# Optimization experiments

Measured on AMD Instinct MI355X. Metric: run time of the kernel, lower is better.

## Reference

```python
import jax, jax.numpy as jnp
import numpy as np

H, D, CR, SEL_K = 8, 64, 32, 16          # query heads, head dim, block size, top-k blocks
ROPE_DIM, THETA, WINDOW, GROUPS = 32, 10000.0, 512, 2
INTER, HID, QC = 512, 1024, 256
NEG = -1e30


def _rope_cache(t):
    half = ROPE_DIM // 2
    inv = 1.0 / (THETA ** (jnp.arange(half, dtype=jnp.float32) * 2.0 / ROPE_DIM))
    ang = jnp.arange(t, dtype=jnp.float32)[:, None] * inv[None, :]  # (t, half)
    return jnp.cos(ang), jnp.sin(ang)


def _apply_partial_rope(x, cos, sin):
    half = ROPE_DIM // 2
    x1, x2, rest = x[..., :half], x[..., half:ROPE_DIM], x[..., ROPE_DIM:]
    return jnp.concatenate([x1 * cos - x2 * sin, x1 * sin + x2 * cos, rest], -1)


def _rmsnorm(x, g, eps=1e-6):
    return x * jax.lax.rsqrt(jnp.mean(x * x, -1, keepdims=True) + eps) * g


def setup_inputs():
    key = jax.random.key(0)
    ks = jax.random.split(key, 9)
    f = lambda k, shp, s: jax.random.normal(k, shp, jnp.float32) * s
    return {
        "h": f(ks[0], (1, 2048, HID), 1.0),
        "w_qc": f(ks[1], (HID, QC), QC ** -0.5),
        "w_qup": f(ks[2], (QC, H * D), (H * D) ** -0.5),
        "w_k": f(ks[3], (HID, D), HID ** -0.5),
        "w_v": f(ks[4], (HID, D), HID ** -0.5),
        "g_qnorm": jnp.ones((D,), jnp.float32),
        "g_knorm": jnp.ones((D,), jnp.float32),
        "w_gate": f(ks[5], (D, 3), 0.05),
        "b_gate": jnp.zeros((3,), jnp.float32),
        "sink_logit": f(ks[6], (H,), 0.1),
        "w_out_group": f(ks[7], (GROUPS, (H // GROUPS) * D, INTER), 0.05),
        "w_out": f(ks[8], (GROUPS * INTER, HID), 0.03),
    }


def reference(h, w_qc, w_qup, w_k, w_v, g_qnorm, g_knorm, w_gate, b_gate,
              sink_logit, w_out_group, w_out):
    b, t, _ = h.shape
    cos, sin = _rope_cache(t)
    q = (h @ w_qc @ w_qup).reshape(b, t, H, D).transpose(0, 2, 1, 3)  # (b,H,t,D)
    q = _rmsnorm(_apply_partial_rope(q, cos, sin), g_qnorm)
    k = _rmsnorm(_apply_partial_rope(h @ w_k, cos, sin), g_knorm)      # (b,t,D)
    v = h @ w_v                                                        # (b,t,D)
    scale = 1.0 / np.sqrt(D).astype(np.float32)
    qpos = jnp.arange(t)
    sink = jnp.broadcast_to(sink_logit[None, :, None, None], (b, H, t, 1))

    # ---- compressed branch: attend over block-mean pooled K/V ----
    nb = t // CR
    kc = k[:, :nb * CR].reshape(b, nb, CR, D).mean(2)                  # (b,nb,D)
    vc = v[:, :nb * CR].reshape(b, nb, CR, D).mean(2)
    comp_valid = ((jnp.arange(nb) + 1) * CR - 1)[None, :] <= qpos[:, None]  # (t,nb)
    any_blk = comp_valid.any(-1, keepdims=True)                        # (t,1)
    safe = jnp.where(any_blk, comp_valid, True)
    sc_raw = jnp.einsum('bhqd,bnd->bhqn', q, kc) * scale
    pc = jax.nn.softmax(jnp.concatenate([jnp.where(safe, sc_raw, NEG), sink], -1), -1)
    comp_out = jnp.einsum('bhqn,bnd->bhqd', pc[..., :nb], vc)
    comp_out = jnp.where(any_blk[None, None], comp_out, 0.0)

    # ---- selective branch: top-k blocks per query, dense-masked gather-equivalent ----
    sel_sc = jnp.where(comp_valid, sc_raw, -jnp.inf)
    top_idx = jax.lax.top_k(sel_sc, min(SEL_K, nb))[1]                 # (b,H,t,K)
    sel_blocks = (top_idx[..., :, None] == jnp.arange(nb)).any(-2)     # (b,H,t,nb)
    block_of = jnp.minimum(qpos // CR, nb - 1)
    causal = qpos[:, None] >= qpos[None, :]                            # (t,t)
    in_range = qpos < nb * CR
    tok_sel = sel_blocks[..., block_of] & (causal & in_range[None, :])[None, None]
    scores_full = jnp.einsum('bhqd,bkd->bhqk', q, k) * scale           # (b,H,t,t)
    ps = jax.nn.softmax(jnp.where(tok_sel, scores_full, NEG), -1)
    sel_out = jnp.einsum('bhqk,bkd->bhqd', ps, v)

    # ---- sliding-window branch ----
    sw = causal & ((qpos[:, None] - qpos[None, :]) < WINDOW)
    pw = jax.nn.softmax(
        jnp.concatenate([jnp.where(sw[None, None], scores_full, NEG), sink], -1), -1)
    sw_out = jnp.einsum('bhqk,bkd->bhqd', pw[..., :t], v)

    # ---- learned gate over the three branches ----
    g = jax.nn.sigmoid(q @ w_gate + b_gate)                            # (b,H,t,3)
    g = g / jnp.clip(g.sum(-1, keepdims=True), 1e-6)
    mixed = g[..., 0:1] * comp_out + g[..., 1:2] * sel_out + g[..., 2:3] * sw_out

    # ---- grouped output projection ----
    x = mixed.transpose(0, 2, 1, 3).reshape(b, t, GROUPS, (H // GROUPS) * D)
    y = jnp.einsum('btgf,gfi->btgi', x, w_out_group).reshape(b, t, GROUPS * INTER)
    return y @ w_out
```

## Files before the change

### kernel.cpp

```cpp
#include <hip/hip_runtime.h>
#include <hip/hip_bf16.h>
#include <float.h>
#include <math.h>

typedef __hip_bfloat16 bf16;
typedef float v2f __attribute__((ext_vector_type(2)));

#define NEGBIG (-1e30f)

__device__ __forceinline__ float ldv(const float* p, int i) { return p[i]; }

__device__ __forceinline__ float wave_sum(float v) {
#pragma unroll
  for (int off = 32; off; off >>= 1) v += __shfl_xor(v, off, 64);
  return v;
}
__device__ __forceinline__ float wave_max(float v) {
#pragma unroll
  for (int off = 32; off; off >>= 1) v = fmaxf(v, __shfl_xor(v, off, 64));
  return v;
}

__device__ __forceinline__ float rdlane(float v, int l) {
  return __uint_as_float(__builtin_amdgcn_readlane(__float_as_uint(v), l));
}

template <int L0>
__device__ __forceinline__ void pv16(const float* __restrict__ vp, float e,
                                     float& a0, float& a1, float& a2, float& a3) {
#pragma unroll
  for (int t = 0; t < 16; t += 4) {
    float p0 = rdlane(e, L0 + t + 0);
    float p1 = rdlane(e, L0 + t + 1);
    float p2 = rdlane(e, L0 + t + 2);
    float p3 = rdlane(e, L0 + t + 3);
    a0 += p0 * vp[(t + 0) * 64];
    a1 += p1 * vp[(t + 1) * 64];
    a2 += p2 * vp[(t + 2) * 64];
    a3 += p3 * vp[(t + 3) * 64];
  }
}

__device__ __forceinline__ float qk_dot(const float4* __restrict__ qr,
                                        const float4* __restrict__ kp) {
  v2f d01 = {0.f, 0.f}, d23 = {0.f, 0.f};
#pragma unroll 1
  for (int i = 0; i < 16; i += 2) {
    float4 q0 = qr[i],     k0 = kp[i * 32];
    float4 q1 = qr[i + 1], k1 = kp[i * 32 + 32];
    d01 += (v2f){q0.x, q0.y} * (v2f){k0.x, k0.y};
    d23 += (v2f){q0.z, q0.w} * (v2f){k0.z, k0.w};
    d01 += (v2f){q1.x, q1.y} * (v2f){k1.x, k1.y};
    d23 += (v2f){q1.z, q1.w} * (v2f){k1.z, k1.w};
  }
  v2f d = d01 + d23;
  return d.x + d.y;
}

__device__ __forceinline__ void gemm_core(
    const float* __restrict__ A, const float* __restrict__ B, float* __restrict__ C,
    int K, int lda, int ldb, int ldc, int row0, int col0)
{
  __shared__ __align__(16) float As[2][16][68];
  __shared__ __align__(16) float Bs[2][16][68];
  const int tid = threadIdx.x;
  const int tx = tid & 15, ty = tid >> 4;
  const int ar = tid >> 2;
  const int ak = (tid & 3) * 4;
  const int bk = tid >> 4;
  const int bc = (tid & 15) * 4;

  const int nk = K >> 4;
  float4 a4 = *reinterpret_cast<const float4*>(&A[(row0 + ar) * lda + ak]);
  float4 b4 = *reinterpret_cast<const float4*>(&B[bk * ldb + col0 + bc]);
  {
    As[0][ak + 0][ar] = a4.x; As[0][ak + 1][ar] = a4.y;
    As[0][ak + 2][ar] = a4.z; As[0][ak + 3][ar] = a4.w;
    *reinterpret_cast<float4*>(&Bs[0][bk][bc]) = b4;
  }

  v2f acc01[4] = {};
  v2f acc23[4] = {};
  for (int t = 0; t < nk; ++t) {
    const int cur = t & 1;
    if (t + 1 < nk) {
      int k0 = (t + 1) * 16;
      a4 = *reinterpret_cast<const float4*>(&A[(row0 + ar) * lda + k0 + ak]);
      b4 = *reinterpret_cast<const float4*>(&B[(k0 + bk) * ldb + col0 + bc]);
    }
    __syncthreads();
#pragma unroll
    for (int kk = 0; kk < 16; ++kk) {
      float4 av = *reinterpret_cast<const float4*>(&As[cur][kk][ty * 4]);
      float4 bv = *reinterpret_cast<const float4*>(&Bs[cur][kk][tx * 4]);
      v2f b01; b01.x = bv.x; b01.y = bv.y;
      v2f b23; b23.x = bv.z; b23.y = bv.w;
      float a[4] = {av.x, av.y, av.z, av.w};
#pragma unroll
      for (int i = 0; i < 4; ++i) {
        v2f as; as.x = a[i]; as.y = a[i];
        acc01[i] += as * b01;
        acc23[i] += as * b23;
      }
    }
    if (t + 1 < nk) {
      const int nxt = cur ^ 1;
      As[nxt][ak + 0][ar] = a4.x; As[nxt][ak + 1][ar] = a4.y;
      As[nxt][ak + 2][ar] = a4.z; As[nxt][ak + 3][ar] = a4.w;
      *reinterpret_cast<float4*>(&Bs[nxt][bk][bc]) = b4;
    }
  }
#pragma unroll
  for (int i = 0; i < 4; ++i) {
    float4 o = make_float4(acc01[i].x, acc01[i].y, acc23[i].x, acc23[i].y);
    *reinterpret_cast<float4*>(&C[(row0 + ty * 4 + i) * ldc + col0 + tx * 4]) = o;
  }
}

__global__ __launch_bounds__(256) void gemm_tile(
    const float* __restrict__ A, const float* __restrict__ B, float* __restrict__ C,
    int M, int N, int K, int lda, int ldb, int ldc)
{
  gemm_core(A, B, C, K, lda, ldb, ldc, blockIdx.y * 64, blockIdx.x * 64);
}

__global__ __launch_bounds__(256) void gemm_qckv(
    const float* __restrict__ h, const float* __restrict__ w_qc,
    const float* __restrict__ w_k, const float* __restrict__ w_v,
    float* __restrict__ hc, float* __restrict__ kb, float* __restrict__ vb)
{
  const int x = blockIdx.x;
  if (x < 4) {
    gemm_core(h, w_qc, hc, 1024, 1024, 256, 256, blockIdx.y * 64, x * 64);
  } else if (x == 4) {
    gemm_core(h, w_k, kb, 1024, 1024, 64, 64, blockIdx.y * 64, 0);
  } else {
    gemm_core(h, w_v, vb, 1024, 1024, 64, 64, blockIdx.y * 64, 0);
  }
}

__global__ __launch_bounds__(256) void gemm_dual(
    const float* __restrict__ A0, const float* __restrict__ A1,
    const float* __restrict__ B0, const float* __restrict__ B1,
    float* __restrict__ C0, float* __restrict__ C1,
    int K, int lda, int ldb, int ldc, int nx)
{
  const bool second = (int)blockIdx.x >= nx;
  const float* A = second ? A1 : A0;
  const float* B = second ? B1 : B0;
  float* C = second ? C1 : C0;
  const int bx = second ? (blockIdx.x - nx) : blockIdx.x;
  gemm_core(A, B, C, K, lda, ldb, ldc, blockIdx.y * 64, bx * 64);
}

__global__ __launch_bounds__(256) void rope_table_kernel(float* __restrict__ ct,
                                                         float* __restrict__ st) {
  int tid = blockIdx.x * 256 + threadIdx.x;
  if (tid >= 2048 * 16) return;
  int pos = tid >> 4, i = tid & 15;
  double ang = (double)pos * pow(10000.0, -(double)i / 16.0);
  ct[tid] = (float)cos(ang);
  st[tid] = (float)sin(ang);
}

__device__ __forceinline__ void rope_body(
    float* __restrict__ x, const float* __restrict__ g, int rows, int posShift,
    float* __restrict__ kS, const float* __restrict__ ct, const float* __restrict__ st,
    int bx)
{
  const int lane = threadIdx.x & 63;
  const int wid = threadIdx.x >> 6;
  const int r = bx * 4 + wid;
  if (r >= rows) return;
  const int pos = r >> posShift;
  float val = x[r * 64 + lane];
  float p = __shfl_xor(val, 16, 64);
  float out = val;
  if (lane < 32) {
    int i = lane & 15;
    float cc = ct[pos * 16 + i], ss = st[pos * 16 + i];
    out = (lane < 16) ? (val * cc - p * ss) : (p * ss + val * cc);
  }
  float ms = wave_sum(out * out) * (1.0f / 64.0f);
  float rn = rsqrtf(ms + 1e-6f);
  float res = out * rn * ldv(g, lane);
  x[r * 64 + lane] = res;
  if (kS) {
    int f4 = (r >> 5) * 512 + (lane >> 2) * 32 + (r & 31);
    kS[f4 * 4 + (lane & 3)] = res;
  }
}

__global__ __launch_bounds__(256) void rope_rms_fused(
    float* __restrict__ qx, float* __restrict__ kx,
    const float* __restrict__ gq, const float* __restrict__ gk,
    float* __restrict__ kS, const float* __restrict__ ct, const float* __restrict__ st)
{
  const int bx = blockIdx.x;
  if (bx < 4096) rope_body(qx, gq, 16384, 3, nullptr, ct, st, bx);
  else           rope_body(kx, gk, 2048, 0, kS, ct, st, bx - 4096);
}

__global__ void compress_kernel(const float* __restrict__ k, const float* __restrict__ v,
                                float* __restrict__ kcT4, float* __restrict__ vc)
{
  const int n = blockIdx.x;
  const int d = threadIdx.x;
  float sk = 0.f, sv = 0.f;
  for (int j = 0; j < 32; ++j) {
    sk += k[(n * 32 + j) * 64 + d];
    sv += v[(n * 32 + j) * 64 + d];
  }
  kcT4[(d >> 2) * 256 + n * 4 + (d & 3)] = sk * (1.0f / 32.0f);
  vc[n * 64 + d] = sv * (1.0f / 32.0f);
}

__global__ __launch_bounds__(512) void attn_kernel(
    const float* __restrict__ q, const float* __restrict__ kS, const float* __restrict__ vbuf,
    const float* __restrict__ kcT4, const float* __restrict__ vc,
    const float* __restrict__ w_gate, const float* __restrict__ b_gate,
    const float* __restrict__ sink, float* __restrict__ mixed)
{
  __shared__ __align__(16) float4 stgK[1024];
  __shared__ __align__(16) float stgV[4096];
  __shared__ __align__(16) float shq[8][64];
  __shared__ int shsel[8][16];
  const int tid = threadIdx.x;
  const int lane = tid & 63;
  const int wid = tid >> 6;
  const int qpos = 2047 - blockIdx.x;
  const int h = wid;
  const int r = qpos * 8 + h;
  const float scale = 0.125f;

  float qv = q[r * 64 + lane];
  shq[wid][lane] = qv;

  float z0 = qv * ldv(w_gate, lane * 3 + 0);
  float z1 = qv * ldv(w_gate, lane * 3 + 1);
  float z2 = qv * ldv(w_gate, lane * 3 + 2);
  z0 = wave_sum(z0) + ldv(b_gate, 0);
  z1 = wave_sum(z1) + ldv(b_gate, 1);
  z2 = wave_sum(z2) + ldv(b_gate, 2);
  float ga0 = 1.f / (1.f + expf(-z0));
  float ga1 = 1.f / (1.f + expf(-z1));
  float ga2 = 1.f / (1.f + expf(-z2));
  float gs = fmaxf(ga0 + ga1 + ga2, 1e-6f);
  float ginv = 1.f / gs;
  ga0 *= ginv; ga1 *= ginv; ga2 *= ginv;

  const float4* qr = reinterpret_cast<const float4*>(&shq[wid][0]);
  const float4* ks4 = reinterpret_cast<const float4*>(kS);
  const float4* kct = reinterpret_cast<const float4*>(kcT4);
  const float snk = ldv(sink, h);
  const int nv = (qpos + 1) >> 5;


  float sc;
  {
    float d0 = 0.f, d1 = 0.f;
#pragma unroll 1
    for (int i = 0; i < 16; i += 2) {
      float4 q0 = qr[i],     k0 = kct[i * 64 + lane];
      float4 q1 = qr[i + 1], k1 = kct[(i + 1) * 64 + lane];
      d0 += q0.x * k0.x + q0.z * k0.z;
      d1 += q0.y * k0.y + q0.w * k0.w;
      d0 += q1.x * k1.x + q1.z * k1.z;
      d1 += q1.y * k1.y + q1.w * k1.w;
    }
    sc = (d0 + d1) * scale;
  }

  float comp_out = 0.f;
  if (nv > 0) {
    float scomp = (lane < nv) ? sc : NEGBIG;
    float m = fmaxf(wave_max(scomp), snk);
    float e = (lane < nv) ? expf(sc - m) : 0.f;
    float S = wave_sum(e) + expf(snk - m);
    float pn = e / S;
    const float* vcp = vc + lane;
    float c0 = 0.f, c1 = 0.f, c2 = 0.f, c3 = 0.f;
    pv16<0>(vcp, pn, c0, c1, c2, c3);
    pv16<16>(vcp + 1024, pn, c0, c1, c2, c3);
    pv16<32>(vcp + 2048, pn, c0, c1, c2, c3);
    pv16<48>(vcp + 3072, pn, c0, c1, c2, c3);
    comp_out = (c0 + c1) + (c2 + c3);
  }

  {
    float selv = (lane < nv) ? sc : -FLT_MAX;
#pragma unroll
    for (int it = 0; it < 16; ++it) {
      float bv = selv; int bi = lane;
#pragma unroll
      for (int off = 32; off; off >>= 1) {
        float ov = __shfl_xor(bv, off, 64);
        int oi = __shfl_xor(bi, off, 64);
        if (ov > bv || (ov == bv && oi < bi)) { bv = ov; bi = oi; }
      }
      if (lane == 0) shsel[wid][it] = bi;
      if (lane == bi) selv = -INFINITY;
    }
  }

  float M = NEGBIG, S = 0.f, osel = 0.f;
#pragma unroll 1
  for (int c = 0; c < 8; ++c) {
    int b0 = shsel[wid][2 * c], b1 = shsel[wid][2 * c + 1];
    int base0 = b0 * 32, base1 = b1 * 32;
    if (base0 > qpos && base1 > qpos) continue;
    int myb = (lane < 32) ? b0 : b1;
    int tok = myb * 32 + (lane & 31);
    bool ok = (tok <= qpos);
    const float4* kp = ks4 + myb * 512 + (lane & 31);
    float s = ok ? qk_dot(qr, kp) * scale : NEGBIG;
    float Mn = fmaxf(M, wave_max(s));
    float e = ok ? expf(s - Mn) : 0.f;
    float cs = wave_sum(e);
    float corr = expf(M - Mn);
    S = S * corr + cs;
    const float* v0 = vbuf + base0 * 64 + lane;
    const float* v1 = vbuf + base1 * 64 + lane;
    float a0 = 0.f, a1 = 0.f, a2 = 0.f, a3 = 0.f;
    pv16<0>(v0, e, a0, a1, a2, a3);
    pv16<16>(v0 + 1024, e, a0, a1, a2, a3);
    pv16<32>(v1, e, a0, a1, a2, a3);
    pv16<48>(v1 + 1024, e, a0, a1, a2, a3);
    osel = osel * corr + ((a0 + a1) + (a2 + a3));
    M = Mn;
  }
  osel /= S;

  float Mw = NEGBIG, Sw = 0.f, osw = 0.f;
  int kstart = qpos - 511; if (kstart < 0) kstart = 0;
  int sbf = kstart >> 5, sbl = qpos >> 5;
  const float4* vbuf4 = reinterpret_cast<const float4*>(vbuf);
#pragma unroll 1
  for (int sb = sbf; sb <= sbl; sb += 2) {
    int sb1 = sb + 1;
    bool v1ok = (sb1 <= sbl);
    int sb1c = v1ok ? sb1 : sb;
    __syncthreads();
#pragma unroll
    for (int j = 0; j < 2; ++j) {
      int g = j * 512 + tid;
      int blk = (g >> 9) ? sb1c : sb;
      stgK[g] = ks4[blk * 512 + (g & 511)];
    }
#pragma unroll
    for (int j = 0; j < 2; ++j) {
      int g = j * 512 + tid;
      int row = g >> 4;
      int srow = (row < 32) ? (sb * 32 + row) : (sb1c * 32 + (row - 32));
      reinterpret_cast<float4*>(stgV)[g] = vbuf4[srow * 16 + (g & 15)];
    }
    __syncthreads();
    int myoff = (lane < 32) ? 0 : 512;
    int tok = ((lane < 32) ? sb : sb1c) * 32 + (lane & 31);
    bool ok = (tok >= kstart) && (tok <= qpos) && ((lane < 32) || v1ok);
    const float4* kp = stgK + myoff + (lane & 31);
    float s = ok ? qk_dot(qr, kp) * scale : NEGBIG;
    float Mn = fmaxf(Mw, wave_max(s));
    float e = ok ? expf(s - Mn) : 0.f;
    float cs = wave_sum(e);
    float corr = expf(Mw - Mn);
    Sw = Sw * corr + cs;
    const float* v0 = stgV + lane;
    const float* v1 = stgV + 2048 + lane;
    float a0 = 0.f, a1 = 0.f, a2 = 0.f, a3 = 0.f;
    pv16<0>(v0, e, a0, a1, a2, a3);
    pv16<16>(v0 + 1024, e, a0, a1, a2, a3);
    pv16<32>(v1, e, a0, a1, a2, a3);
    pv16<48>(v1 + 1024, e, a0, a1, a2, a3);
    osw = osw * corr + ((a0 + a1) + (a2 + a3));
    Mw = Mn;
  }
  {
    float Mf = fmaxf(Mw, snk);
    float corr = expf(Mw - Mf);
    float Sf = Sw * corr + expf(snk - Mf);
    osw = osw * corr / Sf;
  }

  mixed[r * 64 + lane] = ga0 * comp_out + ga1 * osel + ga2 * osw;
}

extern "C" void kernel_launch(void* const* d_in, const int* in_sizes, int n_in,
                              void* d_out, int out_size, void* d_ws, size_t ws_size,
                              hipStream_t stream) {
  const float* h      = (const float*)d_in[0];
  const float* w_qc   = (const float*)d_in[1];
  const float* w_qup  = (const float*)d_in[2];
  const float* w_k    = (const float*)d_in[3];
  const float* w_v    = (const float*)d_in[4];
  const float* g_qn   = (const float*)d_in[5];
  const float* g_kn   = (const float*)d_in[6];
  const float* w_gate = (const float*)d_in[7];
  const float* b_gate = (const float*)d_in[8];
  const float* sink   = (const float*)d_in[9];
  const float* wog    = (const float*)d_in[10];
  const float* w_out  = (const float*)d_in[11];
  float* out = (float*)d_out;

  float* ws = (float*)d_ws;
  float* hc  = ws;
  float* qb  = hc + 2048 * 256;
  float* kb  = qb + 2048 * 512;
  float* vb  = kb + 2048 * 64;
  float* vc  = vb + 2048 * 64;
  float* mx  = vc + 64 * 64;
  float* y1  = mx + 2048 * 512;
  float* kS  = y1 + 2048 * 1024;
  float* kct4 = kS + 2048 * 64;
  float* ct  = kct4 + 16 * 64 * 4;
  float* st  = ct + 2048 * 16;

  dim3 blk(256);
  rope_table_kernel<<<dim3(128), blk, 0, stream>>>(ct, st);
  gemm_qckv<<<dim3(6, 32), blk, 0, stream>>>(h, w_qc, w_k, w_v, hc, kb, vb);
  gemm_tile<<<dim3(8, 32), blk, 0, stream>>>(hc, w_qup, qb, 2048, 512, 256, 256, 512, 512);
  rope_rms_fused<<<dim3(4608), blk, 0, stream>>>(qb, kb, g_qn, g_kn, kS, ct, st);
  compress_kernel<<<dim3(64), dim3(64), 0, stream>>>(kb, vb, kct4, vc);
  attn_kernel<<<dim3(2048), dim3(512), 0, stream>>>(qb, kS, vb, kct4, vc, w_gate, b_gate, sink, mx);
  gemm_dual<<<dim3(16, 32), blk, 0, stream>>>(mx, mx + 256, wog, wog + 256 * 512,
                                              y1, y1 + 512, 256, 512, 512, 1024, 8);
  gemm_tile<<<dim3(16, 32), blk, 0, stream>>>(y1, w_out, out, 2048, 1024, 1024, 1024, 1024, 1024);
}
```

Measured before the change: 417.2 us.

## Run final output projection on bf16 MFMA with pre-transposed weights

The grouped projection now writes its intermediate in bf16, and the final 2048x1024x1024 projection uses bf16 MFMA 16x16x32 instructions in place of the fp32 SIMT tiled GEMM. A new kernel converts w_out to a transposed bf16 copy each call, reusing the hc workspace once the q-up GEMM has consumed it. This is meant to cut the compute cost of the largest GEMM and halve the intermediate traffic. In exchange it adds a transpose pass with strided writes, loads operands straight from global memory without LDS staging, and lowers precision to bf16.

```diff
diff --git a/kernel.cpp b/kernel.cpp
--- a/kernel.cpp
+++ b/kernel.cpp
@@ -5,10 +5,18 @@
 
 typedef __hip_bfloat16 bf16;
 typedef float v2f __attribute__((ext_vector_type(2)));
+typedef float f32x4 __attribute__((ext_vector_type(4)));
+typedef short bf16x8 __attribute__((ext_vector_type(8)));
 
 #define NEGBIG (-1e30f)
 
 __device__ __forceinline__ float ldv(const float* p, int i) { return p[i]; }
+
+__device__ __forceinline__ unsigned short f2bf(float x) {
+  unsigned u = __float_as_uint(x);
+  u += 0x7FFFu + ((u >> 16) & 1u);
+  return (unsigned short)(u >> 16);
+}
 
 __device__ __forceinline__ float wave_sum(float v) {
 #pragma unroll
@@ -57,8 +65,9 @@
   return d.x + d.y;
 }
 
-__device__ __forceinline__ void gemm_core(
-    const float* __restrict__ A, const float* __restrict__ B, float* __restrict__ C,
+template <bool BF16OUT>
+__device__ __forceinline__ void gemm_core_t(
+    const float* __restrict__ A, const float* __restrict__ B, void* __restrict__ Cv,
     int K, int lda, int ldb, int ldc, int row0, int col0)
 {
   __shared__ __align__(16) float As[2][16][68];
@@ -112,8 +121,19 @@
   }
 #pragma unroll
   for (int i = 0; i < 4; ++i) {
-    float4 o = make_float4(acc01[i].x, acc01[i].y, acc23[i].x, acc23[i].y);
-    *reinterpret_cast<float4*>(&C[(row0 + ty * 4 + i) * ldc + col0 + tx * 4]) = o;
+    if (BF16OUT) {
+      unsigned short h0 = f2bf(acc01[i].x), h1 = f2bf(acc01[i].y);
+      unsigned short h2 = f2bf(acc23[i].x), h3 = f2bf(acc23[i].y);
+      uint2 pk;
+      pk.x = (unsigned)h0 | ((unsigned)h1 << 16);
+      pk.y = (unsigned)h2 | ((unsigned)h3 << 16);
+      unsigned short* C = (unsigned short*)Cv;
+      *reinterpret_cast<uint2*>(&C[(row0 + ty * 4 + i) * ldc + col0 + tx * 4]) = pk;
+    } else {
+      float* C = (float*)Cv;
+      float4 o = make_float4(acc01[i].x, acc01[i].y, acc23[i].x, acc23[i].y);
+      *reinterpret_cast<float4*>(&C[(row0 + ty * 4 + i) * ldc + col0 + tx * 4]) = o;
+    }
   }
 }
 
@@ -121,7 +141,7 @@
     const float* __restrict__ A, const float* __restrict__ B, float* __restrict__ C,
     int M, int N, int K, int lda, int ldb, int ldc)
 {
-  gemm_core(A, B, C, K, lda, ldb, ldc, blockIdx.y * 64, blockIdx.x * 64);
+  gemm_core_t<false>(A, B, C, K, lda, ldb, ldc, blockIdx.y * 64, blockIdx.x * 64);
 }
 
 __global__ __launch_bounds__(256) void gemm_qckv(
@@ -131,26 +151,73 @@
 {
   const int x = blockIdx.x;
   if (x < 4) {
-    gemm_core(h, w_qc, hc, 1024, 1024, 256, 256, blockIdx.y * 64, x * 64);
+    gemm_core_t<false>(h, w_qc, hc, 1024, 1024, 256, 256, blockIdx.y * 64, x * 64);
   } else if (x == 4) {
-    gemm_core(h, w_k, kb, 1024, 1024, 64, 64, blockIdx.y * 64, 0);
+    gemm_core_t<false>(h, w_k, kb, 1024, 1024, 64, 64, blockIdx.y * 64, 0);
   } else {
-    gemm_core(h, w_v, vb, 1024, 1024, 64, 64, blockIdx.y * 64, 0);
-  }
-}
-
-__global__ __launch_bounds__(256) void gemm_dual(
+    gemm_core_t<false>(h, w_v, vb, 1024, 1024, 64, 64, blockIdx.y * 64, 0);
+  }
+}
+
+__global__ __launch_bounds__(256) void gemm_dual_b16(
     const float* __restrict__ A0, const float* __restrict__ A1,
     const float* __restrict__ B0, const float* __restrict__ B1,
-    float* __restrict__ C0, float* __restrict__ C1,
+    unsigned short* __restrict__ C0, unsigned short* __restrict__ C1,
     int K, int lda, int ldb, int ldc, int nx)
 {
   const bool second = (int)blockIdx.x >= nx;
   const float* A = second ? A1 : A0;
   const float* B = second ? B1 : B0;
-  float* C = second ? C1 : C0;
+  unsigned short* C = second ? C1 : C0;
   const int bx = second ? (blockIdx.x - nx) : blockIdx.x;
-  gemm_core(A, B, C, K, lda, ldb, ldc, blockIdx.y * 64, bx * 64);
+  gemm_core_t<true>(A, B, C, K, lda, ldb, ldc, blockIdx.y * 64, bx * 64);
+}
+
+__global__ __launch_bounds__(256) void wtrans_kernel(
+    const float* __restrict__ w, unsigned short* __restrict__ wT)
+{
+  int gid = blockIdx.x * 256 + threadIdx.x;
+  int k = gid >> 10, col = gid & 1023;
+  wT[col * 1024 + k] = f2bf(w[k * 1024 + col]);
+}
+
+__global__ __launch_bounds__(256) void gemm_out_mfma(
+    const unsigned short* __restrict__ y1b, const unsigned short* __restrict__ wT,
+    float* __restrict__ out)
+{
+  const int lane = threadIdx.x & 63;
+  const int wid = threadIdx.x >> 6;
+  const int rowbase = blockIdx.y * 64 + wid * 16;
+  const int colbase = blockIdx.x * 64;
+  const int rc = lane & 15;
+  const int kg = lane >> 4;
+  const unsigned short* ap = y1b + (rowbase + rc) * 1024 + kg * 8;
+  const unsigned short* bp = wT + (colbase + rc) * 1024 + kg * 8;
+
+  f32x4 acc0 = {0.f, 0.f, 0.f, 0.f};
+  f32x4 acc1 = {0.f, 0.f, 0.f, 0.f};
+  f32x4 acc2 = {0.f, 0.f, 0.f, 0.f};
+  f32x4 acc3 = {0.f, 0.f, 0.f, 0.f};
+#pragma unroll 2
+  for (int k0 = 0; k0 < 1024; k0 += 32) {
+    bf16x8 a = *reinterpret_cast<const bf16x8*>(ap + k0);
+    bf16x8 b0 = *reinterpret_cast<const bf16x8*>(bp + k0);
+    bf16x8 b1 = *reinterpret_cast<const bf16x8*>(bp + 16 * 1024 + k0);
+    bf16x8 b2 = *reinterpret_cast<const bf16x8*>(bp + 32 * 1024 + k0);
+    bf16x8 b3 = *reinterpret_cast<const bf16x8*>(bp + 48 * 1024 + k0);
+    acc0 = __builtin_amdgcn_mfma_f32_16x16x32_bf16(a, b0, acc0, 0, 0, 0);
+    acc1 = __builtin_amdgcn_mfma_f32_16x16x32_bf16(a, b1, acc1, 0, 0, 0);
+    acc2 = __builtin_amdgcn_mfma_f32_16x16x32_bf16(a, b2, acc2, 0, 0, 0);
+    acc3 = __builtin_amdgcn_mfma_f32_16x16x32_bf16(a, b3, acc3, 0, 0, 0);
+  }
+#pragma unroll
+  for (int j = 0; j < 4; ++j) {
+    int row = rowbase + kg * 4 + j;
+    out[row * 1024 + colbase + rc]      = acc0[j];
+    out[row * 1024 + colbase + 16 + rc] = acc1[j];
+    out[row * 1024 + colbase + 32 + rc] = acc2[j];
+    out[row * 1024 + colbase + 48 + rc] = acc3[j];
+  }
 }
 
 __global__ __launch_bounds__(256) void rope_table_kernel(float* __restrict__ ct,
@@ -254,7 +321,6 @@
   const float4* kct = reinterpret_cast<const float4*>(kcT4);
   const float snk = ldv(sink, h);
   const int nv = (qpos + 1) >> 5;
-
 
   float sc;
   {
@@ -415,14 +481,18 @@
   float* ct  = kct4 + 16 * 64 * 4;
   float* st  = ct + 2048 * 16;
 
+  unsigned short* y1b = (unsigned short*)y1;
+  unsigned short* wT  = (unsigned short*)hc;
+
   dim3 blk(256);
   rope_table_kernel<<<dim3(128), blk, 0, stream>>>(ct, st);
   gemm_qckv<<<dim3(6, 32), blk, 0, stream>>>(h, w_qc, w_k, w_v, hc, kb, vb);
   gemm_tile<<<dim3(8, 32), blk, 0, stream>>>(hc, w_qup, qb, 2048, 512, 256, 256, 512, 512);
+  wtrans_kernel<<<dim3(4096), blk, 0, stream>>>(w_out, wT);
   rope_rms_fused<<<dim3(4608), blk, 0, stream>>>(qb, kb, g_qn, g_kn, kS, ct, st);
   compress_kernel<<<dim3(64), dim3(64), 0, stream>>>(kb, vb, kct4, vc);
   attn_kernel<<<dim3(2048), dim3(512), 0, stream>>>(qb, kS, vb, kct4, vc, w_gate, b_gate, sink, mx);
-  gemm_dual<<<dim3(16, 32), blk, 0, stream>>>(mx, mx + 256, wog, wog + 256 * 512,
-                                              y1, y1 + 512, 256, 512, 512, 1024, 8);
-  gemm_tile<<<dim3(16, 32), blk, 0, stream>>>(y1, w_out, out, 2048, 1024, 1024, 1024, 1024, 1024);
-}
+  gemm_dual_b16<<<dim3(16, 32), blk, 0, stream>>>(mx, mx + 256, wog, wog + 256 * 512,
+                                                  y1b, y1b + 512, 256, 512, 512, 1024, 8);
+  gemm_out_mfma<<<dim3(16, 32), blk, 0, stream>>>(y1b, wT, out);
+}
```

Measured after the change: 399.5 us. -4.2%, faster.
